# Optimization experiments

Measured on AMD Instinct MI355X. Metric: run time of the kernel, lower is better.

Reference implementation:

```python
import jax, jax.numpy as jnp
import numpy as np

DIM = 192
HEADS = 4
EPS_LN = 1e-5
EPS_NORM = 1e-12


def _layernorm(x, w, b):
    # x: [b, c, h, w]; normalize over channel dim (equiv to 'b (h w) c' LN over last axis)
    mu = jnp.mean(x, axis=1, keepdims=True)
    var = jnp.mean((x - mu) ** 2, axis=1, keepdims=True)
    return (x - mu) / jnp.sqrt(var + EPS_LN) * w[None, :, None, None] + b[None, :, None, None]


def _conv1x1(x, w):
    # w: [out_c, in_c]
    return jnp.einsum('bchw,oc->bohw', x, w)


def _dwconv3x3(x, w):
    # w: [c, 1, 3, 3], depthwise (groups = c), padding 1
    return jax.lax.conv_general_dilated(
        x, w, window_strides=(1, 1), padding='SAME',
        feature_group_count=x.shape[1],
        dimension_numbers=('NCHW', 'OIHW', 'NCHW'))


def _l2norm(x):
    # F.normalize(dim=-1): x / max(||x||_2, eps)
    n = jnp.sqrt(jnp.sum(x * x, axis=-1, keepdims=True))
    return x / jnp.maximum(n, EPS_NORM)


def setup_inputs() -> dict:
    key = jax.random.key(0)
    ks = jax.random.split(key, 10)
    b, c, h, w = 8, DIM, 128, 128
    inp = {
        'xx': jax.random.normal(ks[0], (b, c, h, w), jnp.float32),
        'q_in': jax.random.normal(ks[1], (b, c, h, w), jnp.float32),
        'ln_w': jnp.ones((c,), jnp.float32),
        'ln_b': jnp.zeros((c,), jnp.float32),
        'w_q': jax.random.normal(ks[2], (c, c), jnp.float32) * 0.02,
        'w_k': jax.random.normal(ks[3], (c, c), jnp.float32) * 0.02,
        'w_v': jax.random.normal(ks[4], (c, c), jnp.float32) * 0.02,
        'wd_q': jax.random.normal(ks[5], (c, 1, 3, 3), jnp.float32) * 0.1,
        'wd_k': jax.random.normal(ks[6], (c, 1, 3, 3), jnp.float32) * 0.1,
        'wd_v': jax.random.normal(ks[7], (c, 1, 3, 3), jnp.float32) * 0.1,
        'w_proj': jax.random.normal(ks[8], (c, c), jnp.float32) * 0.02,
        'temperature': jnp.ones((HEADS, 1, 1), jnp.float32),
    }
    return inp


def reference(xx, q_in, ln_w, ln_b, w_q, w_k, w_v, wd_q, wd_k, wd_v, w_proj, temperature):
    b, c, h, w = xx.shape
    hw = h * w
    dh = c // HEADS  # per-head channel dim

    x_n = _layernorm(xx, ln_w, ln_b)
    q_n = _layernorm(q_in, ln_w, ln_b)

    q = _dwconv3x3(_conv1x1(q_n, w_q), wd_q)
    k = _dwconv3x3(_conv1x1(x_n, w_k), wd_k)
    v = _dwconv3x3(_conv1x1(x_n, w_v), wd_v)

    # b (head c) h w -> b head c (h w)
    q = q.reshape(b, HEADS, dh, hw)
    k = k.reshape(b, HEADS, dh, hw)
    v = v.reshape(b, HEADS, dh, hw)

    q = _l2norm(q)
    k = _l2norm(k)

    # channel-channel attention: [b, head, dh, dh]
    attn = jnp.einsum('bhcn,bhdn->bhcd', q, k) * temperature[None]
    attn = jax.nn.softmax(attn, axis=-1)

    out = jnp.einsum('bhcd,bhdn->bhcn', attn, v)  # [b, head, dh, hw]
    out = out.reshape(b, c, h, w)
    out = _conv1x1(out, w_proj) + q_in
    return out
```

## Files before the change

### kernel.cpp

```cpp
#include <hip/hip_runtime.h>
#include <hip/hip_bf16.h>
#include <stdint.h>

#define HWSZ 16384
#define CCH 192
#define NB 8
#define NHEAD 4
#define DHEAD 48

typedef unsigned short u16;
typedef __bf16 bf16x8 __attribute__((ext_vector_type(8)));
typedef float f32x4 __attribute__((ext_vector_type(4)));
typedef short s16x8 __attribute__((ext_vector_type(8)));
typedef short s16x4 __attribute__((ext_vector_type(4)));

__device__ __forceinline__ float b2f(u16 h){
  union { unsigned u; float f; } v; v.u = ((unsigned)h) << 16; return v.f;
}
__device__ __forceinline__ u16 f2b(float f){
  union { float f; unsigned u; } v; v.f = f;
  unsigned r = v.u + 0x7fffu + ((v.u >> 16) & 1u);
  return (u16)(r >> 16);
}

__global__ __launch_bounds__(256) void k_wpack(
    const float* __restrict__ wq, const float* __restrict__ wk,
    const float* __restrict__ wv, u16* __restrict__ o)
{
  int m = blockIdx.x;
  const float* src = (m == 0) ? wq : (m == 1) ? wk : wv;
  u16* dst = o + (size_t)m * CCH * CCH;
  int tid = threadIdx.x;
  #pragma unroll
  for (int i = 0; i < 36; ++i){
    int e = (i * 256 + tid) * 4;
    float4 v = *(const float4*)(src + e);
    s16x4 pk;
    pk[0] = (short)f2b(v.x); pk[1] = (short)f2b(v.y);
    pk[2] = (short)f2b(v.z); pk[3] = (short)f2b(v.w);
    *(s16x4*)(dst + e) = pk;
  }
}

template<int NG>
__global__ __launch_bounds__(256) void k_lngemm(
    const float* __restrict__ x, const float* __restrict__ lnw,
    const float* __restrict__ lnb,
    const u16* __restrict__ W0, const u16* __restrict__ W1,
    u16* __restrict__ O0, u16* __restrict__ O1)
{
  __shared__ float xs[CCH * 66];
  __shared__ float red[512];
  __shared__ u16 lnX[64 * 200];
  int tid = threadIdx.x;
  int b   = blockIdx.y;
  int p0  = blockIdx.x * 64;

  float wl = 0.f, bl = 0.f;
  if (tid >= 64){
    int c = tid - 64;
    wl = lnw[c]; bl = lnb[c];
  }

  {
    const float* xb = x + (size_t)b * CCH * HWSZ + p0;
    int cq = tid >> 4;
    int q  = tid & 15;
    float4 v[12];
    #pragma unroll
    for (int i = 0; i < 12; ++i){
      int c = i * 16 + cq;
      v[i] = *(const float4*)(xb + (size_t)c * HWSZ + q * 4);
    }
    #pragma unroll
    for (int i = 0; i < 12; ++i){
      int c = i * 16 + cq;
      float* dst = &xs[c * 66 + q * 4];
      *(float2*)(dst)     = make_float2(v[i].x, v[i].y);
      *(float2*)(dst + 2) = make_float2(v[i].z, v[i].w);
    }
  }
  __syncthreads();

  {
    int w = tid >> 6, l = tid & 63;
    float s = 0.f, ss = 0.f;
    #pragma unroll
    for (int j = 0; j < 48; ++j){
      float v = xs[(48 * w + j) * 66 + l];
      s += v; ss += v * v;
    }
    red[w * 64 + l]       = s;
    red[256 + w * 64 + l] = ss;
  }
  __syncthreads();

  float mu = 0.f, rs = 0.f;
  if (tid < 64){
    float s  = red[tid]       + red[64 + tid]  + red[128 + tid] + red[192 + tid];
    float ss = red[256 + tid] + red[320 + tid] + red[384 + tid] + red[448 + tid];
    mu = s * (1.f / CCH);
    float var = ss * (1.f / CCH) - mu * mu;
    rs = rsqrtf(var + 1e-5f);
  }
  __syncthreads();
  if (tid < 64){ red[tid] = mu; red[64 + tid] = rs; }
  else { int c = tid - 64; red[128 + c] = wl; red[320 + c] = bl; }
  __syncthreads();

  {
    int px = tid >> 2;
    int cb = tid & 3;
    float m = red[px];
    float r = red[64 + px];
    #pragma unroll
    for (int i = 0; i < 6; ++i){
      int c0 = (cb + i * 4) * 8;
      s16x8 pk;
      #pragma unroll
      for (int j = 0; j < 8; ++j){
        int c = c0 + j;
        float o = (xs[c * 66 + px] - m) * r * red[128 + c] + red[320 + c];
        pk[j] = (short)f2b(o);
      }
      *(s16x8*)(&lnX[px * 200 + c0]) = pk;
    }
  }
  __syncthreads();

  int lane = tid & 63, wid = tid >> 6;
  int quad = lane >> 4, r = lane & 15;
  int wm = wid * 48;
  const u16* A0 = W0 + (size_t)wm * CCH;
  const u16* A1 = (NG == 2) ? (W1 + (size_t)wm * CCH) : nullptr;
  f32x4 acc0[3][4] = {};
  f32x4 acc1[3][4] = {};
  #pragma unroll
  for (int ks = 0; ks < 6; ++ks){
    int k0 = ks * 32;
    bf16x8 bfv[4];
    #pragma unroll
    for (int j = 0; j < 4; ++j)
      bfv[j] = *(const bf16x8*)(&lnX[(j * 16 + r) * 200 + k0 + quad * 8]);
    bf16x8 a0[3], a1[3];
    #pragma unroll
    for (int i = 0; i < 3; ++i)
      a0[i] = *(const bf16x8*)(A0 + (size_t)(i * 16 + r) * CCH + k0 + quad * 8);
    if (NG == 2){
      #pragma unroll
      for (int i = 0; i < 3; ++i)
        a1[i] = *(const bf16x8*)(A1 + (size_t)(i * 16 + r) * CCH + k0 + quad * 8);
    }
    #pragma unroll
    for (int i = 0; i < 3; ++i)
      #pragma unroll
      for (int j = 0; j < 4; ++j)
        acc0[i][j] = __builtin_amdgcn_mfma_f32_16x16x32_bf16(a0[i], bfv[j], acc0[i][j], 0, 0, 0);
    if (NG == 2){
      #pragma unroll
      for (int i = 0; i < 3; ++i)
        #pragma unroll
        for (int j = 0; j < 4; ++j)
          acc1[i][j] = __builtin_amdgcn_mfma_f32_16x16x32_bf16(a1[i], bfv[j], acc1[i][j], 0, 0, 0);
    }
  }
  size_t ob = (size_t)b * CCH * HWSZ;
  #pragma unroll
  for (int i = 0; i < 3; ++i){
    #pragma unroll
    for (int rg = 0; rg < 4; ++rg){
      int o = wm + i * 16 + quad * 4 + rg;
      size_t rowb = ob + (size_t)o * HWSZ;
      #pragma unroll
      for (int j = 0; j < 4; ++j){
        int n = p0 + j * 16 + r;
        O0[rowb + n] = f2b(acc0[i][j][rg]);
        if (NG == 2) O1[rowb + n] = f2b(acc1[i][j][rg]);
      }
    }
  }
}

__global__ __launch_bounds__(256) void k_dw3(
    const float* __restrict__ wq, const float* __restrict__ wk,
    const float* __restrict__ wv,
    u16* __restrict__ bq, u16* __restrict__ bk, u16* __restrict__ bv,
    float* __restrict__ ssq_q, float* __restrict__ ssq_k)
{
  int tid = threadIdx.x;
  int bc  = blockIdx.x;
  int z   = blockIdx.y;
  int c   = bc % CCH;
  const float* wd = (z == 0) ? wq : (z == 1) ? wk : wv;
  u16* buf = (z == 0) ? bq : (z == 1) ? bk : bv;
  float w[9];
  #pragma unroll
  for (int t = 0; t < 9; ++t) w[t] = wd[c * 9 + t];
  u16* p = buf + (size_t)bc * HWSZ;

  int xseg = tid & 15, ygrp = tid >> 4;
  int x0 = xseg * 8, y0 = ygrp * 8;

  s16x8 zz = {0,0,0,0,0,0,0,0};
  s16x8 raw[10];
  #pragma unroll
  for (int rr = 0; rr < 10; ++rr){
    int yy = y0 - 1 + rr;
    raw[rr] = (yy >= 0 && yy < 128) ? *(const s16x8*)(p + yy * 128 + x0) : zz;
  }
  __syncthreads();

  float cf[10][8];
  float lf[10], rgt[10];
  #pragma unroll
  for (int rr = 0; rr < 10; ++rr){
    #pragma unroll
    for (int j = 0; j < 8; ++j) cf[rr][j] = b2f((u16)raw[rr][j]);
    float l  = __shfl_up(cf[rr][7], 1);
    float rr_ = __shfl_down(cf[rr][0], 1);
    lf[rr]  = (xseg > 0)  ? l   : 0.f;
    rgt[rr] = (xseg < 15) ? rr_ : 0.f;
  }

  float ss = 0.f;
  #pragma unroll
  for (int k = 0; k < 8; ++k){
    float acc[8] = {0.f,0.f,0.f,0.f,0.f,0.f,0.f,0.f};
    #pragma unroll
    for (int dy = 0; dy < 3; ++dy){
      int rr = k + dy;
      float wl = w[dy * 3], wc = w[dy * 3 + 1], wr = w[dy * 3 + 2];
      acc[0] += wl * lf[rr] + wc * cf[rr][0] + wr * cf[rr][1];
      #pragma unroll
      for (int j = 1; j < 7; ++j)
        acc[j] += wl * cf[rr][j - 1] + wc * cf[rr][j] + wr * cf[rr][j + 1];
      acc[7] += wl * cf[rr][6] + wc * cf[rr][7] + wr * rgt[rr];
    }
    s16x8 pk;
    #pragma unroll
    for (int j = 0; j < 8; ++j){
      pk[j] = (short)f2b(acc[j]);
      ss += acc[j] * acc[j];
    }
    *(s16x8*)(p + (y0 + k) * 128 + x0) = pk;
  }

  if (z < 2){
    #pragma unroll
    for (int m = 32; m > 0; m >>= 1) ss += __shfl_xor(ss, m);
    if ((tid & 63) == 0) atomicAdd(&((z == 0) ? ssq_q : ssq_k)[bc], ss);
  }
}

__global__ void k_gram(const u16* __restrict__ q, const u16* __restrict__ k,
                       float* __restrict__ G)
{
  __shared__ float gs[4 * 48 * 49];
  int tid = threadIdx.x;
  int chunk = blockIdx.x;
  int h = blockIdx.y, b = blockIdx.z;
  int lane = tid & 63, w = tid >> 6;
  int quad = lane >> 4, r = lane & 15;
  int nb = chunk * 1024 + w * 256;
  const u16* qb = q + ((size_t)b * CCH + h * DHEAD) * HWSZ;
  const u16* kb = k + ((size_t)b * CCH + h * DHEAD) * HWSZ;
  f32x4 acc[3][3] = {};
  for (int s = 0; s < 8; ++s){
    int kk = nb + s * 32 + quad * 8;
    bf16x8 af[3], bfr[3];
    #pragma unroll
    for (int i = 0; i < 3; ++i){
      af[i]  = *(const bf16x8*)(qb + (size_t)(i * 16 + r) * HWSZ + kk);
      bfr[i] = *(const bf16x8*)(kb + (size_t)(i * 16 + r) * HWSZ + kk);
    }
    #pragma unroll
    for (int i = 0; i < 3; ++i)
      #pragma unroll
      for (int j = 0; j < 3; ++j)
        acc[i][j] = __builtin_amdgcn_mfma_f32_16x16x32_bf16(af[i], bfr[j], acc[i][j], 0, 0, 0);
  }
  float* gw = gs + w * (48 * 49);
  #pragma unroll
  for (int i = 0; i < 3; ++i)
    #pragma unroll
    for (int j = 0; j < 3; ++j)
      #pragma unroll
      for (int rg = 0; rg < 4; ++rg){
        int row = i * 16 + quad * 4 + rg;
        int col = j * 16 + r;
        gw[row * 49 + col] = acc[i][j][rg];
      }
  __syncthreads();
  float* gb = G + (size_t)(b * NHEAD + h) * (DHEAD * DHEAD);
  #pragma unroll
  for (int t = 0; t < 9; ++t){
    int e = t * 256 + tid;
    int row = e / 48, col = e - row * 48;
    int o = row * 49 + col;
    float s = gs[o] + gs[48 * 49 + o] + gs[2 * 48 * 49 + o] + gs[3 * 48 * 49 + o];
    atomicAdd(&gb[e], s);
  }
}

__global__ __launch_bounds__(256) void k_mk(
    const float* __restrict__ G, const float* __restrict__ ssq_q,
    const float* __restrict__ ssq_k, const float* __restrict__ temp,
    const float* __restrict__ wp, u16* __restrict__ Mout)
{
  __shared__ u16 Pt[48 * 72];
  __shared__ u16 wA[192 * 72];
  __shared__ float rks[48];
  int tid = threadIdx.x;
  int h = blockIdx.x, b = blockIdx.y;
  {
    s16x8 z = {};
    #pragma unroll
    for (int i = 0; i < 2; ++i){
      int idx = (i * 256 + tid) * 8;
      if (idx < 48 * 72) *(s16x8*)(&Pt[idx]) = z;
    }
    #pragma unroll
    for (int i = 0; i < 7; ++i){
      int idx = (i * 256 + tid) * 8;
      if (idx < 192 * 72) *(s16x8*)(&wA[idx]) = z;
    }
  }
  if (tid < DHEAD)
    rks[tid] = 1.f / fmaxf(sqrtf(ssq_k[b * CCH + h * DHEAD + tid]), 1e-12f);
  __syncthreads();
  if (tid < DHEAD){
    float rq = temp[h] / fmaxf(sqrtf(ssq_q[b * CCH + h * DHEAD + tid]), 1e-12f);
    const float* gr = G + (size_t)(b * NHEAD + h) * (DHEAD * DHEAD) + tid * DHEAD;
    float a[DHEAD];
    float mx = -1e30f;
    #pragma unroll
    for (int d = 0; d < DHEAD; ++d){
      a[d] = gr[d] * rq * rks[d];
      mx = fmaxf(mx, a[d]);
    }
    float sum = 0.f;
    #pragma unroll
    for (int d = 0; d < DHEAD; ++d){ a[d] = __expf(a[d] - mx); sum += a[d]; }
    float inv = 1.f / sum;
    #pragma unroll
    for (int d = 0; d < DHEAD; ++d) Pt[d * 72 + tid] = f2b(a[d] * inv);
  }
  {
    const float* wb = wp + h * DHEAD;
    #pragma unroll
    for (int i = 0; i < 9; ++i){
      int e = (i * 256 + tid) * 4;
      int row = e / DHEAD, col = e - row * DHEAD;
      float4 v = *(const float4*)(wb + (size_t)row * CCH + col);
      s16x4 pk;
      pk[0] = (short)f2b(v.x); pk[1] = (short)f2b(v.y);
      pk[2] = (short)f2b(v.z); pk[3] = (short)f2b(v.w);
      *(s16x4*)(&wA[row * 72 + col]) = pk;
    }
  }
  __syncthreads();
  int lane = tid & 63, wid = tid >> 6;
  int quad = lane >> 4, r = lane & 15;
  int wm = wid * 48;
  f32x4 acc[3][3] = {};
  #pragma unroll
  for (int ks = 0; ks < 2; ++ks){
    int k0 = ks * 32;
    bf16x8 af[3], bf[3];
    #pragma unroll
    for (int i = 0; i < 3; ++i)
      af[i] = *(const bf16x8*)(&wA[(wm + i * 16 + r) * 72 + k0 + quad * 8]);
    #pragma unroll
    for (int j = 0; j < 3; ++j)
      bf[j] = *(const bf16x8*)(&Pt[(j * 16 + r) * 72 + k0 + quad * 8]);
    #pragma unroll
    for (int i = 0; i < 3; ++i)
      #pragma unroll
      for (int j = 0; j < 3; ++j)
        acc[i][j] = __builtin_amdgcn_mfma_f32_16x16x32_bf16(af[i], bf[j], acc[i][j], 0, 0, 0);
  }
  u16* mb = Mout + (size_t)b * (CCH * CCH) + h * DHEAD;
  #pragma unroll
  for (int i = 0; i < 3; ++i)
    #pragma unroll
    for (int j = 0; j < 3; ++j)
      #pragma unroll
      for (int rg = 0; rg < 4; ++rg){
        int o = wm + i * 16 + quad * 4 + rg;
        int d = j * 16 + r;
        mb[(size_t)o * CCH + d] = f2b(acc[i][j][rg]);
      }
}

__global__ __launch_bounds__(256) void k_gemmv(
    const u16* __restrict__ M, const u16* __restrict__ V,
    float* __restrict__ Out, const float* __restrict__ resid)
{
  __shared__ u16 lA[64 * 200];
  __shared__ u16 lV[96 * 264];
  int tid = threadIdx.x;
  int n0 = blockIdx.x * 128;
  int m0 = blockIdx.y * 64;
  int b  = blockIdx.z;
  {
    const u16* ap = M + (size_t)b * (CCH * CCH) + m0 * CCH;
    #pragma unroll
    for (int i = 0; i < 6; ++i){
      int off = (i * 256 + tid) * 8;
      int row = off / CCH, col = off - row * CCH;
      *(int4*)(&lA[row * 200 + col]) = *(const int4*)(ap + off);
    }
  }
  {
    const u16* vp = V + (size_t)b * CCH * HWSZ + n0;
    #pragma unroll
    for (int i = 0; i < 12; ++i){
      int e = i * 256 + tid;
      int c = e >> 4, ns = (e & 15) * 8;
      int4 v = *(const int4*)(vp + (size_t)c * HWSZ + ns);
      int kb = c >> 5, kr = c & 31;
      int tile = (kr >> 2) & 1;
      int mr = ((kr >> 3) << 2) | (kr & 3);
      int ti = (kb * 8 + (ns >> 4)) * 2 + tile;
      *(int4*)(&lV[ti * 264 + mr * 16 + (ns & 15)]) = v;
    }
  }
  __syncthreads();
  int lane = tid & 63, wid = tid >> 6;
  int quad = lane >> 4, r = lane & 15;
  int wm = (wid >> 1) * 32, wn = (wid & 1) * 64;
  unsigned lvb = (unsigned)(uintptr_t)(&lV[0]) + 2u * (unsigned)(r + quad * 64)
               + (unsigned)((wn >> 4) * 2) * 528u;
  f32x4 acc[2][4] = {};
  #pragma unroll
  for (int kb = 0; kb < 6; ++kb){
    int k0 = kb * 32;
    s16x4 lo[4], hi[4];
    #pragma unroll
    for (int j = 0; j < 4; ++j){
      unsigned a = lvb + (unsigned)kb * 8448u + (unsigned)j * 1056u;
      asm volatile("ds_read_b64_tr_b16 %0, %1" : "=&v"(lo[j]) : "v"(a));
      asm volatile("ds_read_b64_tr_b16 %0, %1 offset:528" : "=&v"(hi[j]) : "v"(a));
    }
    bf16x8 af[2];
    #pragma unroll
    for (int i = 0; i < 2; ++i)
      af[i] = *(const bf16x8*)(&lA[(wm + i * 16 + r) * 200 + k0 + quad * 8]);
    asm volatile("s_waitcnt lgkmcnt(0)" ::: "memory");
    __builtin_amdgcn_sched_barrier(0);
    #pragma unroll
    for (int j = 0; j < 4; ++j){
      union { s16x8 s; bf16x8 b; } u;
      u.s = __builtin_shufflevector(lo[j], hi[j], 0, 1, 2, 3, 4, 5, 6, 7);
      #pragma unroll
      for (int i = 0; i < 2; ++i)
        acc[i][j] = __builtin_amdgcn_mfma_f32_16x16x32_bf16(af[i], u.b, acc[i][j], 0, 0, 0);
    }
  }
  size_t obase = (size_t)b * CCH * HWSZ;
  #pragma unroll
  for (int i = 0; i < 2; ++i){
    #pragma unroll
    for (int rg = 0; rg < 4; ++rg){
      int o = m0 + wm + i * 16 + quad * 4 + rg;
      size_t rowb = obase + (size_t)o * HWSZ;
      #pragma unroll
      for (int j = 0; j < 4; ++j){
        int n = n0 + wn + j * 16 + r;
        Out[rowb + n] = acc[i][j][rg] + resid[rowb + n];
      }
    }
  }
}

extern "C" void kernel_launch(void* const* d_in, const int* in_sizes, int n_in,
                              void* d_out, int out_size, void* d_ws, size_t ws_size,
                              hipStream_t stream)
{
  const float* xx     = (const float*)d_in[0];
  const float* q_in   = (const float*)d_in[1];
  const float* ln_w   = (const float*)d_in[2];
  const float* ln_b   = (const float*)d_in[3];
  const float* w_q    = (const float*)d_in[4];
  const float* w_k    = (const float*)d_in[5];
  const float* w_v    = (const float*)d_in[6];
  const float* wd_q   = (const float*)d_in[7];
  const float* wd_k   = (const float*)d_in[8];
  const float* wd_v   = (const float*)d_in[9];
  const float* w_proj = (const float*)d_in[10];
  const float* temp   = (const float*)d_in[11];

  const size_t SZ = (size_t)NB * CCH * HWSZ;
  u16* B1 = (u16*)d_ws;
  u16* B2 = B1 + SZ;
  u16* B3 = B2 + SZ;
  float* G     = (float*)(B3 + SZ);
  float* ssq_q = G + 32 * DHEAD * DHEAD;
  float* ssq_k = ssq_q + NB * CCH;
  u16* Mb      = (u16*)(ssq_k + NB * CCH);
  u16* Wb      = Mb + (size_t)NB * CCH * CCH;

  hipMemsetAsync(G, 0, (size_t)(32 * DHEAD * DHEAD + 2 * NB * CCH) * sizeof(float), stream);

  k_wpack<<<3, 256, 0, stream>>>(w_q, w_k, w_v, Wb);
  k_lngemm<2><<<dim3(256, NB), 256, 0, stream>>>(
      xx, ln_w, ln_b, Wb + CCH * CCH, Wb + 2 * CCH * CCH, B2, B1);
  k_lngemm<1><<<dim3(256, NB), 256, 0, stream>>>(
      q_in, ln_w, ln_b, Wb, nullptr, B3, nullptr);
  k_dw3<<<dim3(NB * CCH, 3), 256, 0, stream>>>(wd_q, wd_k, wd_v,
                                               B3, B2, B1, ssq_q, ssq_k);
  k_gram<<<dim3(16, NHEAD, NB), 256, 0, stream>>>(B3, B2, G);
  k_mk<<<dim3(NHEAD, NB), 256, 0, stream>>>(G, ssq_q, ssq_k, temp, w_proj, Mb);
  k_gemmv<<<dim3(128, 3, NB), 256, 0, stream>>>(Mb, B1, (float*)d_out, q_in);
}
```

Before: 433.5 us.

## Compute layernorm stats from registers and feed MFMA via transposed LDS reads

The layernorm+GEMM kernel no longer stages the full fp32 input tile in shared memory. Statistics are reduced directly from the loaded registers, and normalized bf16 values are written channel-major into a tiled LDS layout. The MFMA B operand is then fetched with ds_read_b64_tr_b16 transposing loads. This cuts LDS footprint and traffic and removes a sync, which may raise occupancy, but it relies on inline asm, a manual waitcnt and intricate index math.

```diff
diff --git a/kernel.cpp b/kernel.cpp
--- a/kernel.cpp
+++ b/kernel.cpp
@@ -49,12 +49,15 @@
     const u16* __restrict__ W0, const u16* __restrict__ W1,
     u16* __restrict__ O0, u16* __restrict__ O1)
 {
-  __shared__ float xs[CCH * 66];
-  __shared__ float red[512];
-  __shared__ u16 lnX[64 * 200];
+  __shared__ u16 lnT[12672];
+  __shared__ float red[2048];
+  __shared__ float mures[128];
+  __shared__ float lwlb[384];
   int tid = threadIdx.x;
   int b   = blockIdx.y;
   int p0  = blockIdx.x * 64;
+  int cq  = tid >> 4;
+  int q   = tid & 15;
 
   float wl = 0.f, bl = 0.f;
   if (tid >= 64){
@@ -62,68 +65,63 @@
     wl = lnw[c]; bl = lnb[c];
   }
 
+  float4 v[12];
   {
     const float* xb = x + (size_t)b * CCH * HWSZ + p0;
-    int cq = tid >> 4;
-    int q  = tid & 15;
-    float4 v[12];
+    #pragma unroll
+    for (int i = 0; i < 12; ++i)
+      v[i] = *(const float4*)(xb + (size_t)(i * 16 + cq) * HWSZ + q * 4);
+  }
+  {
+    float4 ps  = make_float4(0.f, 0.f, 0.f, 0.f);
+    float4 pss = make_float4(0.f, 0.f, 0.f, 0.f);
+    #pragma unroll
+    for (int i = 0; i < 12; ++i){
+      ps.x += v[i].x; ps.y += v[i].y; ps.z += v[i].z; ps.w += v[i].w;
+      pss.x += v[i].x * v[i].x; pss.y += v[i].y * v[i].y;
+      pss.z += v[i].z * v[i].z; pss.w += v[i].w * v[i].w;
+    }
+    *(float4*)(&red[cq * 64 + q * 4])        = ps;
+    *(float4*)(&red[1024 + cq * 64 + q * 4]) = pss;
+  }
+  __syncthreads();
+
+  if (tid < 64){
+    float s = 0.f, ss2 = 0.f;
+    #pragma unroll
+    for (int j = 0; j < 16; ++j){
+      s   += red[j * 64 + tid];
+      ss2 += red[1024 + j * 64 + tid];
+    }
+    float mu  = s * (1.f / CCH);
+    float var = ss2 * (1.f / CCH) - mu * mu;
+    mures[tid]      = mu;
+    mures[64 + tid] = rsqrtf(var + 1e-5f);
+  } else {
+    int c = tid - 64;
+    lwlb[c] = wl; lwlb[192 + c] = bl;
+  }
+  __syncthreads();
+
+  {
+    float m0 = mures[q * 4 + 0], m1 = mures[q * 4 + 1];
+    float m2 = mures[q * 4 + 2], m3 = mures[q * 4 + 3];
+    float r0 = mures[64 + q * 4 + 0], r1 = mures[64 + q * 4 + 1];
+    float r2 = mures[64 + q * 4 + 2], r3 = mures[64 + q * 4 + 3];
     #pragma unroll
     for (int i = 0; i < 12; ++i){
       int c = i * 16 + cq;
-      v[i] = *(const float4*)(xb + (size_t)c * HWSZ + q * 4);
-    }
-    #pragma unroll
-    for (int i = 0; i < 12; ++i){
-      int c = i * 16 + cq;
-      float* dst = &xs[c * 66 + q * 4];
-      *(float2*)(dst)     = make_float2(v[i].x, v[i].y);
-      *(float2*)(dst + 2) = make_float2(v[i].z, v[i].w);
-    }
-  }
-  __syncthreads();
-
-  {
-    int w = tid >> 6, l = tid & 63;
-    float s = 0.f, ss = 0.f;
-    #pragma unroll
-    for (int j = 0; j < 48; ++j){
-      float v = xs[(48 * w + j) * 66 + l];
-      s += v; ss += v * v;
-    }
-    red[w * 64 + l]       = s;
-    red[256 + w * 64 + l] = ss;
-  }
-  __syncthreads();
-
-  float mu = 0.f, rs = 0.f;
-  if (tid < 64){
-    float s  = red[tid]       + red[64 + tid]  + red[128 + tid] + red[192 + tid];
-    float ss = red[256 + tid] + red[320 + tid] + red[384 + tid] + red[448 + tid];
-    mu = s * (1.f / CCH);
-    float var = ss * (1.f / CCH) - mu * mu;
-    rs = rsqrtf(var + 1e-5f);
-  }
-  __syncthreads();
-  if (tid < 64){ red[tid] = mu; red[64 + tid] = rs; }
-  else { int c = tid - 64; red[128 + c] = wl; red[320 + c] = bl; }
-  __syncthreads();
-
-  {
-    int px = tid >> 2;
-    int cb = tid & 3;
-    float m = red[px];
-    float r = red[64 + px];
-    #pragma unroll
-    for (int i = 0; i < 6; ++i){
-      int c0 = (cb + i * 4) * 8;
-      s16x8 pk;
-      #pragma unroll
-      for (int j = 0; j < 8; ++j){
-        int c = c0 + j;
-        float o = (xs[c * 66 + px] - m) * r * red[128 + c] + red[320 + c];
-        pk[j] = (short)f2b(o);
-      }
-      *(s16x8*)(&lnX[px * 200 + c0]) = pk;
+      float lw_ = lwlb[c], lb_ = lwlb[192 + c];
+      s16x4 pk;
+      pk[0] = (short)f2b((v[i].x - m0) * r0 * lw_ + lb_);
+      pk[1] = (short)f2b((v[i].y - m1) * r1 * lw_ + lb_);
+      pk[2] = (short)f2b((v[i].z - m2) * r2 * lw_ + lb_);
+      pk[3] = (short)f2b((v[i].w - m3) * r3 * lw_ + lb_);
+      int kb   = c >> 5, kr = c & 31;
+      int tile = (kr >> 2) & 1;
+      int mr   = ((kr >> 3) << 2) | (kr & 3);
+      int ti   = (kb * 4 + (q >> 2)) * 2 + tile;
+      *(s16x4*)(&lnT[ti * 264 + mr * 16 + (q & 3) * 4]) = pk;
     }
   }
   __syncthreads();
@@ -135,13 +133,10 @@
   const u16* A1 = (NG == 2) ? (W1 + (size_t)wm * CCH) : nullptr;
   f32x4 acc0[3][4] = {};
   f32x4 acc1[3][4] = {};
-  #pragma unroll
-  for (int ks = 0; ks < 6; ++ks){
-    int k0 = ks * 32;
-    bf16x8 bfv[4];
-    #pragma unroll
-    for (int j = 0; j < 4; ++j)
-      bfv[j] = *(const bf16x8*)(&lnX[(j * 16 + r) * 200 + k0 + quad * 8]);
+  unsigned lvb = (unsigned)(uintptr_t)(&lnT[0]) + 2u * (unsigned)(r + quad * 64);
+  #pragma unroll
+  for (int kb = 0; kb < 6; ++kb){
+    int k0 = kb * 32;
     bf16x8 a0[3], a1[3];
     #pragma unroll
     for (int i = 0; i < 3; ++i)
@@ -151,17 +146,27 @@
       for (int i = 0; i < 3; ++i)
         a1[i] = *(const bf16x8*)(A1 + (size_t)(i * 16 + r) * CCH + k0 + quad * 8);
     }
-    #pragma unroll
-    for (int i = 0; i < 3; ++i)
-      #pragma unroll
-      for (int j = 0; j < 4; ++j)
-        acc0[i][j] = __builtin_amdgcn_mfma_f32_16x16x32_bf16(a0[i], bfv[j], acc0[i][j], 0, 0, 0);
-    if (NG == 2){
+    s16x4 lo[4], hi[4];
+    #pragma unroll
+    for (int j = 0; j < 4; ++j){
+      unsigned a = lvb + (unsigned)kb * 4224u + (unsigned)j * 1056u;
+      asm volatile("ds_read_b64_tr_b16 %0, %1" : "=&v"(lo[j]) : "v"(a));
+      asm volatile("ds_read_b64_tr_b16 %0, %1 offset:528" : "=&v"(hi[j]) : "v"(a));
+    }
+    asm volatile("s_waitcnt lgkmcnt(0)" ::: "memory");
+    __builtin_amdgcn_sched_barrier(0);
+    #pragma unroll
+    for (int j = 0; j < 4; ++j){
+      union { s16x8 s; bf16x8 b; } u;
+      u.s = __builtin_shufflevector(lo[j], hi[j], 0, 1, 2, 3, 4, 5, 6, 7);
       #pragma unroll
       for (int i = 0; i < 3; ++i)
+        acc0[i][j] = __builtin_amdgcn_mfma_f32_16x16x32_bf16(a0[i], u.b, acc0[i][j], 0, 0, 0);
+      if (NG == 2){
         #pragma unroll
-        for (int j = 0; j < 4; ++j)
-          acc1[i][j] = __builtin_amdgcn_mfma_f32_16x16x32_bf16(a1[i], bfv[j], acc1[i][j], 0, 0, 0);
+        for (int i = 0; i < 3; ++i)
+          acc1[i][j] = __builtin_amdgcn_mfma_f32_16x16x32_bf16(a1[i], u.b, acc1[i][j], 0, 0, 0);
+      }
     }
   }
   size_t ob = (size_t)b * CCH * HWSZ;
```

Measured after the change: 437.6 us. About the same (+0.9%).
